# Optimization experiments

Measured on AMD Instinct MI355X. Metric: run time of the kernel, lower is better.

The kernel has to match this reference:

```python
import jax, jax.numpy as jnp
import numpy as np

B, S, D_IN, H, D_OUT = 2048, 16, 512, 1024, 64

def _lin_init(key, fan_in, fan_out):
    k1, k2 = jax.random.split(key)
    bound = 1.0 / np.sqrt(fan_in)
    W = jax.random.uniform(k1, (fan_in, fan_out), jnp.float32, -bound, bound)
    b = jax.random.uniform(k2, (fan_out,), jnp.float32, -bound, bound)
    return W, b

def setup_inputs() -> dict:
    key = jax.random.key(0)
    ks = jax.random.split(key, 7)
    x = jax.random.normal(ks[0], (B, S, D_IN), jnp.float32)
    Wi, bi = _lin_init(ks[1], D_IN, H)
    W1, b1 = _lin_init(ks[2], H, H)
    W2, b2 = _lin_init(ks[3], H, H)
    W3, b3 = _lin_init(ks[4], H, H)
    Wo1, bo1 = _lin_init(ks[5], H, H // 2)
    Wo2, bo2 = _lin_init(ks[6], H // 2, D_OUT)
    return {"x": x, "Wi": Wi, "bi": bi, "W1": W1, "b1": b1, "W2": W2, "b2": b2,
            "W3": W3, "b3": b3, "Wo1": Wo1, "bo1": bo1, "Wo2": Wo2, "bo2": bo2}

def reference(x, Wi, bi, W1, b1, W2, b2, W3, b3, Wo1, bo1, Wo2, bo2):
    seq_len = x.shape[1]
    dt = 1.0 / (seq_len - 1)  # t = linspace(0, 1, seq_len)

    def f(h):
        h = jax.nn.gelu(h @ W1 + b1, approximate=False)
        h = jax.nn.gelu(h @ W2 + b2, approximate=False)
        h = jax.nn.gelu(h @ W3 + b3, approximate=False)
        return h

    h0 = x[:, 0, :] @ Wi + bi  # [B, H]

    def rk4_38_step(h, _):  # torchdiffeq fixed-grid rk4 uses the 3/8 rule
        k1 = f(h)
        k2 = f(h + dt * k1 / 3.0)
        k3 = f(h + dt * (k2 - k1 / 3.0))
        k4 = f(h + dt * (k1 - k2 + k3))
        return h + dt * (k1 + 3.0 * k2 + 3.0 * k3 + k4) / 8.0, None

    h_final, _ = jax.lax.scan(rk4_38_step, h0, None, length=seq_len - 1)
    out = jax.nn.gelu(h_final @ Wo1 + bo1, approximate=False) @ Wo2 + bo2
    return out
```

## Files before the change

### kernel.cpp

```cpp
#include <hip/hip_runtime.h>
#include <hip/hip_bf16.h>
#include <math.h>

typedef __attribute__((ext_vector_type(8))) short bf16x8;
typedef __attribute__((ext_vector_type(4))) float f32x4;

#define EPI_T   0
#define EPI_H0  1
#define EPI_K1  2
#define EPI_K2  3
#define EPI_K3  4
#define EPI_K4  5
#define EPI_OUT 6

static __device__ __forceinline__ unsigned short f2bf(float f) {
  unsigned int u = __float_as_uint(f);
  u += 0x7FFFu + ((u >> 16) & 1u);
  return (unsigned short)(u >> 16);
}
static __device__ __forceinline__ float bf2f(unsigned short s) {
  return __uint_as_float(((unsigned int)s) << 16);
}
static __device__ __forceinline__ float gelu_f(float x) {
  return 0.5f * x * (1.0f + erff(x * 0.70710678118654752f));
}

typedef __attribute__((address_space(3))) unsigned int lds_u32;
typedef const __attribute__((address_space(1))) unsigned int glb_u32;
static __device__ __forceinline__ void gl_lds16(const unsigned short* g, unsigned short* l) {
  __builtin_amdgcn_global_load_lds((glb_u32*)g, (lds_u32*)l, 16, 0, 0);
}

template<int EPI>
__global__ __launch_bounds__(256)
void gemm_k(const unsigned short* __restrict__ A,
            const unsigned short* __restrict__ Wt,
            const float* __restrict__ bias,
            void* __restrict__ outp,
            unsigned short* __restrict__ ob2,
            const float* __restrict__ hF,
            float* __restrict__ huF,
            const unsigned short* __restrict__ k1p,
            const unsigned short* __restrict__ k2p,
            float dt, int N, int K, int nwg)
{
  __shared__ __attribute__((aligned(16))) unsigned short As[2][64][64];

  const int bid = blockIdx.x;
  const int cpx = nwg >> 3;
  const int wid = (bid & 7) * cpx + (bid >> 3);
  const int nbx = N >> 6;
  const int bx = wid % nbx, by = wid / nbx;
  const int brow = by << 6, bcol = bx << 6;

  const int tid = threadIdx.x;
  const int lane = tid & 63;
  const int wv = tid >> 6;
  const int wr = wv >> 1, wc = wv & 1;
  const int l15 = lane & 15, l4 = lane >> 4;
  const int lr = lane >> 3;
  const int sc = (lane & 7) ^ lr;
  const int KT = K >> 6;

  f32x4 acc[2][2];
  const f32x4 zf = {0.f, 0.f, 0.f, 0.f};
#pragma unroll
  for (int m = 0; m < 2; ++m)
#pragma unroll
    for (int n = 0; n < 2; ++n) acc[m][n] = zf;

  const unsigned short* pB0 = Wt + (size_t)(bcol + wc * 32 + l15) * K + l4 * 8;
  const unsigned short* pB1 = pB0 + (size_t)16 * K;

  auto STAGE = [&](int buf, int kt) {
    const int kof = kt << 6;
#pragma unroll
    for (int c = 0; c < 2; ++c) {
      const int r0 = c * 32 + wv * 8;
      gl_lds16(A + (size_t)(brow + r0 + lr) * K + kof + sc * 8, &As[buf][r0][0]);
    }
  };

  STAGE(0, 0);
  int b = 0;
  for (int kt = 0; kt < KT; ++kt) {
    __syncthreads();
    if (kt + 1 < KT) STAGE(b ^ 1, kt + 1);
    bf16x8 bg0[2], bg1[2];
#pragma unroll
    for (int ks = 0; ks < 2; ++ks) {
      bg0[ks] = *(const bf16x8*)(pB0 + kt * 64 + ks * 32);
      bg1[ks] = *(const bf16x8*)(pB1 + kt * 64 + ks * 32);
    }
#pragma unroll
    for (int ks = 0; ks < 2; ++ks) {
      const int ch = ((ks * 4 + l4) ^ (l15 & 7)) * 8;
      bf16x8 af0 = *(const bf16x8*)&As[b][wr * 32 + l15][ch];
      bf16x8 af1 = *(const bf16x8*)&As[b][wr * 32 + 16 + l15][ch];
      acc[0][0] = __builtin_amdgcn_mfma_f32_16x16x32_bf16(af0, bg0[ks], acc[0][0], 0, 0, 0);
      acc[0][1] = __builtin_amdgcn_mfma_f32_16x16x32_bf16(af0, bg1[ks], acc[0][1], 0, 0, 0);
      acc[1][0] = __builtin_amdgcn_mfma_f32_16x16x32_bf16(af1, bg0[ks], acc[1][0], 0, 0, 0);
      acc[1][1] = __builtin_amdgcn_mfma_f32_16x16x32_bf16(af1, bg1[ks], acc[1][1], 0, 0, 0);
    }
    b ^= 1;
  }

  const float dt3 = dt * (1.f / 3.f), dt8 = dt * 0.125f, dt38 = dt * 0.375f;
#pragma unroll
  for (int n = 0; n < 2; ++n) {
    const int col = bcol + wc * 32 + n * 16 + l15;
    const float bv = bias[col];
#pragma unroll
    for (int m = 0; m < 2; ++m) {
      const int r0 = brow + wr * 32 + m * 16 + l4 * 4;
#pragma unroll
      for (int r = 0; r < 4; ++r) {
        const int row = r0 + r;
        const float a = acc[m][n][r] + bv;
        const size_t ix = (size_t)row * N + col;
        const size_t ih = (size_t)row * 1024 + col;
        if constexpr (EPI == EPI_T) {
          ((unsigned short*)outp)[ix] = f2bf(gelu_f(a));
        } else if constexpr (EPI == EPI_H0) {
          ((float*)outp)[ix] = a;
          ob2[ix] = f2bf(a);
        } else if constexpr (EPI == EPI_K1) {
          const float k1 = gelu_f(a);
          const float h = hF[ih];
          ((unsigned short*)outp)[ih] = f2bf(k1);
          huF[ih] = h + dt8 * k1;
          ob2[ih] = f2bf(h + dt3 * k1);
        } else if constexpr (EPI == EPI_K2) {
          const float k2 = gelu_f(a);
          const float h = hF[ih];
          const float k1 = bf2f(k1p[ih]);
          ((unsigned short*)outp)[ih] = f2bf(k2);
          huF[ih] += dt38 * k2;
          ob2[ih] = f2bf(h - dt3 * k1 + dt * k2);
        } else if constexpr (EPI == EPI_K3) {
          const float k3 = gelu_f(a);
          const float h = hF[ih];
          const float k1 = bf2f(k1p[ih]);
          const float k2 = bf2f(k2p[ih]);
          huF[ih] += dt38 * k3;
          ob2[ih] = f2bf(h + dt * (k1 - k2 + k3));
        } else if constexpr (EPI == EPI_K4) {
          const float k4 = gelu_f(a);
          const float hn = huF[ih] + dt8 * k4;
          ((float*)outp)[ih] = hn;
          ob2[ih] = f2bf(hn);
        } else {
          ((float*)outp)[ix] = a;
        }
      }
    }
  }
}

__global__ void transpose_k(const float* __restrict__ W, unsigned short* __restrict__ Wt,
                            int K, int N) {
  __shared__ float tile[32][33];
  const int n0 = blockIdx.x * 32, k0 = blockIdx.y * 32;
  const int lx = threadIdx.x, ly = threadIdx.y;
#pragma unroll
  for (int r = ly; r < 32; r += 8)
    tile[r][lx] = W[(size_t)(k0 + r) * N + n0 + lx];
  __syncthreads();
#pragma unroll
  for (int r = ly; r < 32; r += 8)
    Wt[(size_t)(n0 + r) * K + k0 + lx] = f2bf(tile[lx][r]);
}

__global__ void convx_k(const float* __restrict__ x, unsigned short* __restrict__ xb) {
  const int r = blockIdx.x;
  const int c = threadIdx.x << 3;
  const float* s = x + (size_t)r * 8192 + c;
  f32x4 u0 = *(const f32x4*)s;
  f32x4 u1 = *(const f32x4*)(s + 4);
  union { unsigned short q[8]; bf16x8 v; } t;
#pragma unroll
  for (int j = 0; j < 4; ++j) { t.q[j] = f2bf(u0[j]); t.q[4 + j] = f2bf(u1[j]); }
  *(bf16x8*)(xb + (size_t)r * 512 + c) = t.v;
}

template<int EPI>
static inline void G(hipStream_t st, const void* A, const unsigned short* Wt,
                     const float* bias, void* out, void* ob2,
                     const float* hF, float* huF,
                     const unsigned short* k1p, const unsigned short* k2p,
                     float dt, int N, int K) {
  const int nwg = (2048 / 64) * (N / 64);
  gemm_k<EPI><<<nwg, 256, 0, st>>>((const unsigned short*)A, Wt, bias, out,
                                   (unsigned short*)ob2, hF, huF, k1p, k2p, dt, N, K, nwg);
}

extern "C" void kernel_launch(void* const* d_in, const int* in_sizes, int n_in,
                              void* d_out, int out_size, void* d_ws, size_t ws_size,
                              hipStream_t stream) {
  const float* x   = (const float*)d_in[0];
  const float* Wi  = (const float*)d_in[1];
  const float* bi  = (const float*)d_in[2];
  const float* W1  = (const float*)d_in[3];
  const float* b1  = (const float*)d_in[4];
  const float* W2  = (const float*)d_in[5];
  const float* b2  = (const float*)d_in[6];
  const float* W3  = (const float*)d_in[7];
  const float* b3  = (const float*)d_in[8];
  const float* Wo1 = (const float*)d_in[9];
  const float* bo1 = (const float*)d_in[10];
  const float* Wo2 = (const float*)d_in[11];
  const float* bo2 = (const float*)d_in[12];

  char* ws = (char*)d_ws;
  unsigned short* Wti  = (unsigned short*)(ws + (0ull  << 20));
  unsigned short* Wt1  = (unsigned short*)(ws + (1ull  << 20));
  unsigned short* Wt2  = (unsigned short*)(ws + (3ull  << 20));
  unsigned short* Wt3  = (unsigned short*)(ws + (5ull  << 20));
  unsigned short* Wto1 = (unsigned short*)(ws + (7ull  << 20));
  unsigned short* Wto2 = (unsigned short*)(ws + (8ull  << 20));
  float*          h    = (float*)(ws + (9ull  << 20));
  float*          hu   = (float*)(ws + (17ull << 20));
  unsigned short* xb   = (unsigned short*)hu;
  unsigned short* k1b  = (unsigned short*)(ws + (25ull << 20));
  unsigned short* o1b  = k1b;
  unsigned short* k2b  = (unsigned short*)(ws + (29ull << 20));
  unsigned short* t1b  = (unsigned short*)(ws + (33ull << 20));
  unsigned short* t2b  = (unsigned short*)(ws + (37ull << 20));
  unsigned short* cA   = (unsigned short*)(ws + (41ull << 20));
  unsigned short* hb   = (unsigned short*)(ws + (45ull << 20));

  dim3 tb(32, 8);
  transpose_k<<<dim3(1024 / 32,  512 / 32), tb, 0, stream>>>(Wi,  Wti,  512, 1024);
  transpose_k<<<dim3(1024 / 32, 1024 / 32), tb, 0, stream>>>(W1,  Wt1, 1024, 1024);
  transpose_k<<<dim3(1024 / 32, 1024 / 32), tb, 0, stream>>>(W2,  Wt2, 1024, 1024);
  transpose_k<<<dim3(1024 / 32, 1024 / 32), tb, 0, stream>>>(W3,  Wt3, 1024, 1024);
  transpose_k<<<dim3( 512 / 32, 1024 / 32), tb, 0, stream>>>(Wo1, Wto1, 1024, 512);
  transpose_k<<<dim3(  64 / 32,  512 / 32), tb, 0, stream>>>(Wo2, Wto2,  512,  64);
  convx_k<<<2048, 64, 0, stream>>>(x, xb);

  const float dt = 1.0f / 15.0f;

  G<EPI_H0>(stream, xb, Wti, bi, h, hb, nullptr, nullptr, nullptr, nullptr, dt, 1024, 512);

  for (int s = 0; s < 15; ++s) {
    G<EPI_T >(stream, hb,  Wt1, b1, t1b, nullptr, nullptr, nullptr, nullptr, nullptr, dt, 1024, 1024);
    G<EPI_T >(stream, t1b, Wt2, b2, t2b, nullptr, nullptr, nullptr, nullptr, nullptr, dt, 1024, 1024);
    G<EPI_K1>(stream, t2b, Wt3, b3, k1b, cA, h, hu, nullptr, nullptr, dt, 1024, 1024);
    G<EPI_T >(stream, cA,  Wt1, b1, t1b, nullptr, nullptr, nullptr, nullptr, nullptr, dt, 1024, 1024);
    G<EPI_T >(stream, t1b, Wt2, b2, t2b, nullptr, nullptr, nullptr, nullptr, nullptr, dt, 1024, 1024);
    G<EPI_K2>(stream, t2b, Wt3, b3, k2b, cA, h, hu, k1b, nullptr, dt, 1024, 1024);
    G<EPI_T >(stream, cA,  Wt1, b1, t1b, nullptr, nullptr, nullptr, nullptr, nullptr, dt, 1024, 1024);
    G<EPI_T >(stream, t1b, Wt2, b2, t2b, nullptr, nullptr, nullptr, nullptr, nullptr, dt, 1024, 1024);
    G<EPI_K3>(stream, t2b, Wt3, b3, nullptr, cA, h, hu, k1b, k2b, dt, 1024, 1024);
    G<EPI_T >(stream, cA,  Wt1, b1, t1b, nullptr, nullptr, nullptr, nullptr, nullptr, dt, 1024, 1024);
    G<EPI_T >(stream, t1b, Wt2, b2, t2b, nullptr, nullptr, nullptr, nullptr, nullptr, dt, 1024, 1024);
    G<EPI_K4>(stream, t2b, Wt3, b3, h, hb, nullptr, hu, nullptr, nullptr, dt, 1024, 1024);
  }

  G<EPI_T  >(stream, hb,  Wto1, bo1, o1b, nullptr, nullptr, nullptr, nullptr, nullptr, dt, 512, 1024);
  G<EPI_OUT>(stream, o1b, Wto2, bo2, d_out, nullptr, nullptr, nullptr, nullptr, nullptr, dt, 64, 512);
}
```

Baseline: 3.993 ms.

## Deepen GEMM K-loop pipeline to three LDS stages with BK=128 and prefetched B

Rewrites the GEMM main loop with a three-slot LDS ring, doubling the K tile to 128 and using a 16-chunk XOR swizzle for A. B fragments are prefetched into alternating register sets one iteration ahead. Explicit vmcnt waits and raw barriers replace __syncthreads, and MFMA sections run at raised wave priority. The goal is to hide global load latency better and halve barrier count, at the cost of more LDS (48KB) and registers, with launch bounds asking for 2 blocks per CU.

```diff
diff --git a/kernel.cpp b/kernel.cpp
--- a/kernel.cpp
+++ b/kernel.cpp
@@ -32,7 +32,7 @@
 }
 
 template<int EPI>
-__global__ __launch_bounds__(256)
+__global__ __launch_bounds__(256, 2)
 void gemm_k(const unsigned short* __restrict__ A,
             const unsigned short* __restrict__ Wt,
             const float* __restrict__ bias,
@@ -44,7 +44,7 @@
             const unsigned short* __restrict__ k2p,
             float dt, int N, int K, int nwg)
 {
-  __shared__ __attribute__((aligned(16))) unsigned short As[2][64][64];
+  __shared__ __attribute__((aligned(16))) unsigned short As[3][64][128];
 
   const int bid = blockIdx.x;
   const int cpx = nwg >> 3;
@@ -58,9 +58,7 @@
   const int wv = tid >> 6;
   const int wr = wv >> 1, wc = wv & 1;
   const int l15 = lane & 15, l4 = lane >> 4;
-  const int lr = lane >> 3;
-  const int sc = (lane & 7) ^ lr;
-  const int KT = K >> 6;
+  const int KT = K >> 7;
 
   f32x4 acc[2][2];
   const f32x4 zf = {0.f, 0.f, 0.f, 0.f};
@@ -72,37 +70,60 @@
   const unsigned short* pB0 = Wt + (size_t)(bcol + wc * 32 + l15) * K + l4 * 8;
   const unsigned short* pB1 = pB0 + (size_t)16 * K;
 
-  auto STAGE = [&](int buf, int kt) {
-    const int kof = kt << 6;
-#pragma unroll
-    for (int c = 0; c < 2; ++c) {
-      const int r0 = c * 32 + wv * 8;
-      gl_lds16(A + (size_t)(brow + r0 + lr) * K + kof + sc * 8, &As[buf][r0][0]);
-    }
-  };
+  const int lrow = lane >> 4;
+  auto STAGE = [&](int slot, int kt) {
+    const int kof = kt << 7;
+#pragma unroll
+    for (int c = 0; c < 4; ++c) {
+      const int r0 = wv * 16 + c * 4;
+      const int sc = l15 ^ ((r0 + lrow) & 15);
+      gl_lds16(A + (size_t)(brow + r0 + lrow) * K + kof + sc * 8, &As[slot][r0][0]);
+    }
+  };
+
+  auto LOADB = [&](bf16x8 (&bg)[2][4], int kt) {
+    const int kof = kt << 7;
+#pragma unroll
+    for (int ks = 0; ks < 4; ++ks) {
+      bg[0][ks] = *(const bf16x8*)(pB0 + kof + ks * 32);
+      bg[1][ks] = *(const bf16x8*)(pB1 + kof + ks * 32);
+    }
+  };
+
+  auto COMP = [&](int slot, bf16x8 (&bg)[2][4]) {
+    __builtin_amdgcn_s_setprio(1);
+#pragma unroll
+    for (int ks = 0; ks < 4; ++ks) {
+      const int ch = ((ks * 4 + l4) ^ l15) * 8;
+      bf16x8 af0 = *(const bf16x8*)&As[slot][wr * 32 + l15][ch];
+      bf16x8 af1 = *(const bf16x8*)&As[slot][wr * 32 + 16 + l15][ch];
+      acc[0][0] = __builtin_amdgcn_mfma_f32_16x16x32_bf16(af0, bg[0][ks], acc[0][0], 0, 0, 0);
+      acc[0][1] = __builtin_amdgcn_mfma_f32_16x16x32_bf16(af0, bg[1][ks], acc[0][1], 0, 0, 0);
+      acc[1][0] = __builtin_amdgcn_mfma_f32_16x16x32_bf16(af1, bg[0][ks], acc[1][0], 0, 0, 0);
+      acc[1][1] = __builtin_amdgcn_mfma_f32_16x16x32_bf16(af1, bg[1][ks], acc[1][1], 0, 0, 0);
+    }
+    __builtin_amdgcn_s_setprio(0);
+  };
+
+  bf16x8 Bp[2][4], Bq[2][4];
 
   STAGE(0, 0);
-  int b = 0;
-  for (int kt = 0; kt < KT; ++kt) {
-    __syncthreads();
-    if (kt + 1 < KT) STAGE(b ^ 1, kt + 1);
-    bf16x8 bg0[2], bg1[2];
-#pragma unroll
-    for (int ks = 0; ks < 2; ++ks) {
-      bg0[ks] = *(const bf16x8*)(pB0 + kt * 64 + ks * 32);
-      bg1[ks] = *(const bf16x8*)(pB1 + kt * 64 + ks * 32);
-    }
-#pragma unroll
-    for (int ks = 0; ks < 2; ++ks) {
-      const int ch = ((ks * 4 + l4) ^ (l15 & 7)) * 8;
-      bf16x8 af0 = *(const bf16x8*)&As[b][wr * 32 + l15][ch];
-      bf16x8 af1 = *(const bf16x8*)&As[b][wr * 32 + 16 + l15][ch];
-      acc[0][0] = __builtin_amdgcn_mfma_f32_16x16x32_bf16(af0, bg0[ks], acc[0][0], 0, 0, 0);
-      acc[0][1] = __builtin_amdgcn_mfma_f32_16x16x32_bf16(af0, bg1[ks], acc[0][1], 0, 0, 0);
-      acc[1][0] = __builtin_amdgcn_mfma_f32_16x16x32_bf16(af1, bg0[ks], acc[1][0], 0, 0, 0);
-      acc[1][1] = __builtin_amdgcn_mfma_f32_16x16x32_bf16(af1, bg1[ks], acc[1][1], 0, 0, 0);
-    }
-    b ^= 1;
+  STAGE(1, 1);
+  LOADB(Bp, 0);
+
+  auto body = [&](int t, bf16x8 (&cur)[2][4], bf16x8 (&nxt)[2][4]) {
+    if (t + 1 < KT) { asm volatile("s_waitcnt vmcnt(4)" ::: "memory"); }
+    else            { asm volatile("s_waitcnt vmcnt(0)" ::: "memory"); }
+    __builtin_amdgcn_s_barrier();
+    __builtin_amdgcn_sched_barrier(0);
+    if (t + 1 < KT) LOADB(nxt, t + 1);
+    COMP(t % 3, cur);
+    if (t + 2 < KT) STAGE((t + 2) % 3, t + 2);
+  };
+
+  for (int t = 0; t < KT; t += 2) {
+    body(t, Bp, Bq);
+    body(t + 1, Bq, Bp);
   }
 
   const float dt3 = dt * (1.f / 3.f), dt8 = dt * 0.125f, dt38 = dt * 0.375f;
```

Result: slower. 4.153 ms (+4.0%).
